# Kernel optimization log

Hardware: AMD Instinct MI355X
Metric: run time of the kernel (lower is better)

The kernel has to match this reference:

```python
import jax, jax.numpy as jnp
import numpy as np

V, E, H, T = 50000, 300, 512, 16   # vocab, embed_dim, hidden_dim, tagset
Hh = H // 2                         # per-direction LSTM hidden
B, S = 128, 128                     # batch (hardcoded in module), seq_len
START, STOP = 14, 15
NEG = -10000.0


def setup_inputs() -> dict:
    key = jax.random.key(0)
    ks = jax.random.split(key, 16)
    n = lambda k, sh: (jax.random.normal(k, sh, dtype=jnp.float32) * 0.1)
    trans = jax.random.normal(ks[12], (T, T), dtype=jnp.float32)
    trans = trans.at[START, :].set(NEG).at[:, STOP].set(NEG)
    return {
        "sentence": jax.random.randint(ks[0], (B, S), 0, V, dtype=jnp.int32),
        "emb": jax.random.normal(ks[1], (V, E), dtype=jnp.float32),
        "Wih_f": n(ks[2], (4 * Hh, E)), "Whh_f": n(ks[3], (4 * Hh, Hh)),
        "bih_f": n(ks[4], (4 * Hh,)),   "bhh_f": n(ks[5], (4 * Hh,)),
        "Wih_b": n(ks[6], (4 * Hh, E)), "Whh_b": n(ks[7], (4 * Hh, Hh)),
        "bih_b": n(ks[8], (4 * Hh,)),   "bhh_b": n(ks[9], (4 * Hh,)),
        "W_out": n(ks[10], (T, H)),     "b_out": n(ks[11], (T,)),
        "trans": trans,
        "h0": jax.random.normal(ks[13], (2, B, Hh), dtype=jnp.float32),
        "c0": jax.random.normal(ks[14], (2, B, Hh), dtype=jnp.float32),
    }


def _lstm_dir(x_sbE, h0, c0, Wih, Whh, bih, bhh):
    """x_sbE: [S,B,E] -> [S,B,Hh]. PyTorch gate order: i,f,g,o."""
    def cell(carry, xt):
        h, c = carry
        g = xt @ Wih.T + bih + h @ Whh.T + bhh
        i, f, gg, o = jnp.split(g, 4, axis=-1)
        c = jax.nn.sigmoid(f) * c + jax.nn.sigmoid(i) * jnp.tanh(gg)
        h = jax.nn.sigmoid(o) * jnp.tanh(c)
        return (h, c), h
    _, hs = jax.lax.scan(cell, (h0, c0), x_sbE)
    return hs


def _viterbi(feats, trans):
    """Batched Viterbi. feats: [B,S,T]. Returns (scores [B], paths [B,S])."""
    init = jnp.full((B, T), NEG, dtype=feats.dtype).at[:, START].set(0.0)

    def step(fv, feat_t):
        # next_tag_var[b, next, prev] = fv[b, prev] + trans[next, prev]
        nxt = fv[:, None, :] + trans[None, :, :]
        bp = jnp.argmax(nxt, axis=-1)              # [B,T]
        fv = jnp.max(nxt, axis=-1) + feat_t        # [B,T]
        return fv, bp

    fv, bps = jax.lax.scan(step, init, jnp.swapaxes(feats, 0, 1))  # bps: [S,B,T]
    term = fv + trans[STOP][None, :]
    best = jnp.argmax(term, axis=-1)               # [B]
    score = jnp.max(term, axis=-1)                 # [B]

    def back(tag, bp_t):
        prev = jnp.take_along_axis(bp_t, tag[:, None], axis=1)[:, 0]
        return prev, tag

    _, path = jax.lax.scan(back, best, bps, reverse=True)  # [S,B]
    return score, jnp.swapaxes(path, 0, 1)


def reference(sentence, emb, Wih_f, Whh_f, bih_f, bhh_f,
              Wih_b, Whh_b, bih_b, bhh_b, W_out, b_out, trans, h0, c0):
    x = emb[sentence]                               # [B,S,E] (frozen embedding)
    x_sbE = jnp.swapaxes(x, 0, 1)                   # [S,B,E]
    h_f = _lstm_dir(x_sbE, h0[0], c0[0], Wih_f, Whh_f, bih_f, bhh_f)
    h_b = _lstm_dir(x_sbE[::-1], h0[1], c0[1], Wih_b, Whh_b, bih_b, bhh_b)[::-1]
    lstm_out = jnp.concatenate([h_f, h_b], axis=-1)  # [S,B,H]
    feats = jnp.swapaxes(lstm_out @ W_out.T + b_out, 0, 1)  # [B,S,T]
    scores, tag_seqs = _viterbi(feats, trans)
    return scores, tag_seqs
```

## Files before the change

### kernel.cpp

```cpp
#include <hip/hip_runtime.h>
#include <math.h>
#include <stdint.h>

#define BB 128
#define SS 128
#define EE 300
#define HH 256
#define G4 1024
#define TT 16
#define NEGV -10000.0f
#define START_TAG 14
#define STOP_TAG 15

typedef float f32x4 __attribute__((ext_vector_type(4)));

__device__ __forceinline__ float sigm(float x) { return 1.0f / (1.0f + expf(-x)); }

__device__ __forceinline__ float4 shfl_xor4(float4 v, int m) {
  float4 r;
  r.x = __shfl_xor(v.x, m); r.y = __shfl_xor(v.y, m);
  r.z = __shfl_xor(v.z, m); r.w = __shfl_xor(v.w, m);
  return r;
}
__device__ __forceinline__ void add4(float4& a, const float4& b) {
  a.x += b.x; a.y += b.y; a.z += b.z; a.w += b.w;
}

__device__ __forceinline__ void load_pairs8(const float* p, f32x4& a, f32x4& b) {
  asm volatile("global_load_dwordx4 %0, %2, off sc0 sc1\n\t"
               "global_load_dwordx4 %1, %2, off offset:16 sc0 sc1\n\t"
               "s_waitcnt vmcnt(0)"
               : "=&v"(a), "=&v"(b) : "v"(p) : "memory");
}

__device__ __forceinline__ void store_pair_llc(float2* p, float h, int stamp) {
  uint64_t bits = ((uint64_t)(uint32_t)stamp << 32) | (uint64_t)__float_as_uint(h);
  __hip_atomic_store((uint64_t*)p, bits, __ATOMIC_RELAXED, __HIP_MEMORY_SCOPE_AGENT);
}

__global__ void k_prep(const float* __restrict__ Wih_f, const float* __restrict__ Whh_f,
                       const float* __restrict__ bih_f, const float* __restrict__ bhh_f,
                       const float* __restrict__ Wih_b, const float* __restrict__ Whh_b,
                       const float* __restrict__ bih_b, const float* __restrict__ bhh_b,
                       float* __restrict__ WihT, float* __restrict__ Whh4,
                       float* __restrict__ bsum, float* __restrict__ hpairz) {
  int id = blockIdx.x * blockDim.x + threadIdx.x;
  const int N1 = 2 * EE * G4;
  const int N2 = 2 * HH * G4;
  const int N3 = 2 * G4;
  const int N4 = 3 * 2 * BB * HH * 2;
  if (id < N1) {
    int d = id / (EE * G4); int r = id % (EE * G4);
    int e = r / G4; int j = r % G4;
    const float* W = d ? Wih_b : Wih_f;
    WihT[id] = W[j * EE + e];
  } else if (id < N1 + N2) {
    int t = id - N1;
    int d = t / (HH * G4); int r = t % (HH * G4);
    int k = r / G4; int q = r % G4; int u = q >> 2; int g = q & 3;
    const float* W = d ? Whh_b : Whh_f;
    Whh4[t] = W[(g * HH + u) * HH + k];
  } else if (id < N1 + N2 + N3) {
    int t = id - N1 - N2;
    int d = t / G4; int j = t % G4;
    bsum[t] = d ? (bih_b[j] + bhh_b[j]) : (bih_f[j] + bhh_f[j]);
  } else if (id < N1 + N2 + N3 + N4) {
    hpairz[id - N1 - N2 - N3] = 0.0f;
  }
}

__global__ void k_xproj(const int* __restrict__ sent, const float* __restrict__ emb,
                        const float* __restrict__ WihT, const float* __restrict__ bsum,
                        float4* __restrict__ xp4) {
  __shared__ __align__(16) float xs[16][EE];
  __shared__ int idxs[16];
  int blk = blockIdx.x;
  int d = blk >> 10;
  int tile = blk & 1023;
  int tid = threadIdx.x;
  if (tid < 16) {
    int sb = tile * 16 + tid;
    int s = sb >> 7, b = sb & 127;
    idxs[tid] = sent[b * SS + s];
  }
  __syncthreads();
  for (int t = tid; t < 16 * 75; t += 256) {
    int i = t / 75, e4 = t % 75;
    ((f32x4*)&xs[i][0])[e4] = ((const f32x4*)(emb + (size_t)idxs[i] * EE))[e4];
  }
  __syncthreads();

  const float* WT = WihT + (size_t)d * EE * G4;
  float acc0[16], acc1[16], acc2[16], acc3[16];
#pragma unroll
  for (int i = 0; i < 16; ++i) { acc0[i] = 0.f; acc1[i] = 0.f; acc2[i] = 0.f; acc3[i] = 0.f; }

  for (int e4 = 0; e4 < 75; ++e4) {
    f32x4 xv[16];
#pragma unroll
    for (int i = 0; i < 16; ++i)
      xv[i] = *(const f32x4*)&xs[i][e4 * 4];
    const float* rowb = WT + (size_t)e4 * 4 * G4;
#pragma unroll
    for (int j = 0; j < 4; ++j) {
      const float* row = rowb + (size_t)j * G4;
      float w0 = row[tid];
      float w1 = row[tid + 256];
      float w2 = row[tid + 512];
      float w3 = row[tid + 768];
#pragma unroll
      for (int i = 0; i < 16; ++i) {
        float x = xv[i][j];
        acc0[i] += w0 * x; acc1[i] += w1 * x; acc2[i] += w2 * x; acc3[i] += w3 * x;
      }
    }
  }
  float b0 = bsum[d * G4 + tid];
  float b1 = bsum[d * G4 + tid + 256];
  float b2 = bsum[d * G4 + tid + 512];
  float b3 = bsum[d * G4 + tid + 768];
#pragma unroll
  for (int i = 0; i < 16; ++i) {
    int sb = tile * 16 + i;
    int s = sb >> 7, b = sb & 127;
    xp4[(((size_t)d * SS + s) * BB + b) * HH + tid] =
        make_float4(acc0[i] + b0, acc1[i] + b1, acc2[i] + b2, acc3[i] + b3);
  }
}

__global__ __launch_bounds__(256, 2) void k_recur(
    const float4* __restrict__ xp4, const float4* __restrict__ Wg,
    const float* __restrict__ h0, const float* __restrict__ c0,
    float2* __restrict__ hpair, float* __restrict__ hall) {
  __shared__ __align__(16) float hsh[2][4 * 288];

  int blk = blockIdx.x;
  int d = blk >> 8;
  int bg = (blk >> 3) & 31;
  int sl = blk & 7;
  int bbase = bg * 4;
  int tid = threadIdx.x;
  int u = tid >> 3, kc = tid & 7;
  int uglob = sl * 32 + u;

  float4 wreg[32];
  {
    const float4* Wd = Wg + (size_t)d * (HH * HH) + (size_t)(kc * 32) * HH + uglob;
#pragma unroll
    for (int kk = 0; kk < 32; ++kk) wreg[kk] = Wd[(size_t)kk * HH];
  }
  int b_own = ((kc & 1) << 1) | ((kc >> 1) & 1);
  float c_reg = c0[((size_t)d * BB + bbase + b_own) * HH + uglob];
  bool up0 = (kc & 1), up1 = (kc & 2);

  int sb = tid >> 6;
  int k4 = (tid & 63) * 4;
  int ldoff = sb * 288 + (k4 >> 5) * 36 + (k4 & 31);

  for (int step = 0; step < SS; ++step) {
    int s = d ? (SS - 1 - step) : step;
    int pb = step & 1;
    float4 xg = xp4[(((size_t)d * SS + s) * BB + bbase + b_own) * HH + uglob];

    float* ldst = &hsh[pb][ldoff];
    if (step == 0) {
      const float* ps = h0 + ((size_t)d * BB + bbase + sb) * HH + k4;
      *(f32x4*)ldst = *(const f32x4*)ps;
    } else {
      int slot_r = (step + 2) % 3;
      const float* ps = (const float*)(hpair +
          ((size_t)(slot_r * 2 + d) * BB + bbase + sb) * HH + k4);
      f32x4 v0, v1;
      load_pairs8(ps, v0, v1);
      while (__float_as_int(v0[1]) != step || __float_as_int(v0[3]) != step ||
             __float_as_int(v1[1]) != step || __float_as_int(v1[3]) != step) {
        __builtin_amdgcn_s_sleep(1);
        load_pairs8(ps, v0, v1);
      }
      f32x4 q = {v0[0], v0[2], v1[0], v1[2]};
      *(f32x4*)ldst = q;
    }
    __syncthreads();

    const float* hb = &hsh[pb][0];
    float4 a[4];
#pragma unroll
    for (int b = 0; b < 4; ++b) a[b] = make_float4(0.f, 0.f, 0.f, 0.f);
#pragma unroll
    for (int kk4 = 0; kk4 < 8; ++kk4) {
      float hvv[4][4];
#pragma unroll
      for (int b = 0; b < 4; ++b)
        *(f32x4*)&hvv[b][0] = *(const f32x4*)&hb[b * 288 + kc * 36 + kk4 * 4];
#pragma unroll
      for (int j = 0; j < 4; ++j) {
        float4 w = wreg[kk4 * 4 + j];
#pragma unroll
        for (int b = 0; b < 4; ++b) {
          float hj = hvv[b][j];
          a[b].x += w.x * hj; a[b].y += w.y * hj;
          a[b].z += w.z * hj; a[b].w += w.w * hj;
        }
      }
    }

#pragma unroll
    for (int j = 0; j < 2; ++j) {
      float4 snd = up0 ? a[j] : a[j + 2];
      float4 rcv = shfl_xor4(snd, 1);
      if (!up0) add4(a[j], rcv); else add4(a[j + 2], rcv);
    }
    float4 v0 = up0 ? a[2] : a[0];
    float4 v1 = up0 ? a[3] : a[1];
    {
      float4 snd = up1 ? v0 : v1;
      float4 rcv = shfl_xor4(snd, 2);
      if (!up1) add4(v0, rcv); else add4(v1, rcv);
    }
    float4 keep = up1 ? v1 : v0;
    {
      float4 rcv = shfl_xor4(keep, 4);
      add4(keep, rcv);
    }

    float ii = keep.x + xg.x, ff = keep.y + xg.y;
    float gg = keep.z + xg.z, oo = keep.w + xg.w;
    c_reg = sigm(ff) * c_reg + sigm(ii) * tanhf(gg);
    float hn = sigm(oo) * tanhf(c_reg);

    if (kc < 4) {
      store_pair_llc(&hpair[((size_t)((step % 3) * 2 + d) * BB + bbase + b_own) * HH + uglob],
                     hn, step + 1);
      hall[(((size_t)d * SS + step) * BB + bbase + b_own) * HH + uglob] = hn;
    }
  }
}

__global__ void k_feats(const float* __restrict__ hall, const float* __restrict__ Wout,
                        float* __restrict__ featsF) {
  __shared__ __align__(16) float h2[16][516];
  int b = blockIdx.x >> 3;
  int sg = blockIdx.x & 7;
  int tid = threadIdx.x;

  for (int i = tid; i < 16 * 128; i += 256) {
    int r = i >> 7, seg = i & 127;
    int s = sg * 16 + r;
    f32x4 v;
    if (seg < 64)
      v = *(const f32x4*)&hall[(((size_t)0 * SS + s) * BB + b) * HH + seg * 4];
    else
      v = *(const f32x4*)&hall[(((size_t)1 * SS + (SS - 1 - s)) * BB + b) * HH + (seg - 64) * 4];
    *(f32x4*)&h2[r][seg * 4] = v;
  }
  __syncthreads();

  int sloc = tid >> 4, t = tid & 15;
  const float* wrow = Wout + t * 512;
  float p = 0.f;
  for (int j = 0; j < 128; ++j) {
    f32x4 hv = *(const f32x4*)&h2[sloc][j * 4];
    f32x4 wv = *(const f32x4*)&wrow[j * 4];
    p += hv[0] * wv[0] + hv[1] * wv[1] + hv[2] * wv[2] + hv[3] * wv[3];
  }
  featsF[((size_t)b * SS + sg * 16 + sloc) * TT + t] = p;
}

__global__ void k_viterbi(const float* __restrict__ featsF, const float* __restrict__ b_out,
                          const float* __restrict__ trans, float* __restrict__ out) {
  __shared__ float tr[TT * TT];
  __shared__ unsigned char bpl[16][SS][TT];
  int tid = threadIdx.x;
  if (tid < TT * TT) tr[tid] = trans[tid];
  __syncthreads();

  int bg = tid >> 4;
  int next = tid & 15;
  int b = blockIdx.x * 16 + bg;
  float fv = (next == START_TAG) ? 0.0f : NEGV;
  float bo = b_out[next];
  const float* fF = featsF + (size_t)b * SS * TT;

  for (int s = 0; s < SS; ++s) {
    float best = -INFINITY; int arg = 0;
#pragma unroll
    for (int prev = 0; prev < TT; ++prev) {
      float fvp = __shfl(fv, prev, 16);
      float cand = fvp + tr[next * TT + prev];
      if (cand > best) { best = cand; arg = prev; }
    }
    float feat = fF[s * TT + next] + bo;
    fv = best + feat;
    bpl[bg][s][next] = (unsigned char)arg;
  }

  float bv = fv + tr[STOP_TAG * TT + next];
  int bi = next;
#pragma unroll
  for (int off = 8; off; off >>= 1) {
    float ov = __shfl_down(bv, off, 16);
    int oi = __shfl_down(bi, off, 16);
    if (ov > bv || (ov == bv && oi < bi)) { bv = ov; bi = oi; }
  }
  if (next == 0) {
    out[b] = bv;
    int tag = bi;
    float* po = out + BB + (size_t)b * SS;
    for (int s = SS - 1; s >= 0; --s) {
      po[s] = (float)tag;
      tag = bpl[bg][s][tag];
    }
  }
}

extern "C" void kernel_launch(void* const* d_in, const int* in_sizes, int n_in,
                              void* d_out, int out_size, void* d_ws, size_t ws_size,
                              hipStream_t stream) {
  const int*   sent  = (const int*)d_in[0];
  const float* emb   = (const float*)d_in[1];
  const float* Wih_f = (const float*)d_in[2];
  const float* Whh_f = (const float*)d_in[3];
  const float* bih_f = (const float*)d_in[4];
  const float* bhh_f = (const float*)d_in[5];
  const float* Wih_b = (const float*)d_in[6];
  const float* Whh_b = (const float*)d_in[7];
  const float* bih_b = (const float*)d_in[8];
  const float* bhh_b = (const float*)d_in[9];
  const float* Wout  = (const float*)d_in[10];
  const float* b_out = (const float*)d_in[11];
  const float* trans = (const float*)d_in[12];
  const float* h0    = (const float*)d_in[13];
  const float* c0    = (const float*)d_in[14];

  float* ws = (float*)d_ws;
  size_t off = 0;
  float* xproj  = ws + off; off += (size_t)2 * SS * BB * G4;
  float* WihT   = ws + off; off += (size_t)2 * EE * G4;
  float* Whh4   = ws + off; off += (size_t)2 * HH * G4;
  float* bsum   = ws + off; off += (size_t)2 * G4;
  float* featsF = ws + off; off += (size_t)BB * SS * TT;
  float* hall   = ws + off; off += (size_t)2 * SS * BB * HH;
  float* hpairf = ws + off; off += (size_t)3 * 2 * BB * HH * 2;

  const int NPREP = 2 * EE * G4 + 2 * HH * G4 + 2 * G4 + 3 * 2 * BB * HH * 2;
  k_prep<<<(NPREP + 255) / 256, 256, 0, stream>>>(Wih_f, Whh_f, bih_f, bhh_f,
                                                  Wih_b, Whh_b, bih_b, bhh_b,
                                                  WihT, Whh4, bsum, hpairf);
  k_xproj<<<2048, 256, 0, stream>>>(sent, emb, WihT, bsum, (float4*)xproj);

  {
    const float4* xp4c = (const float4*)xproj;
    const float4* Wgc  = (const float4*)Whh4;
    float2* hpair = (float2*)hpairf;
    void* kargs[] = {(void*)&xp4c, (void*)&Wgc, (void*)&h0, (void*)&c0,
                     (void*)&hpair, (void*)&hall};
    hipError_t e = hipLaunchCooperativeKernel(k_recur, dim3(512), dim3(256),
                                              kargs, 0, stream);
    if (e != hipSuccess) {
      k_recur<<<512, 256, 0, stream>>>(xp4c, Wgc, h0, c0, hpair, hall);
    }
  }

  k_feats<<<1024, 256, 0, stream>>>(hall, Wout, featsF);
  k_viterbi<<<8, 256, 0, stream>>>(featsF, b_out, trans, (float*)d_out);
}
```

Before: 909.0 us.

## Fuse input projection into recurrence kernel with per-row stamp flags for overlap

Merges the embedding/input-projection kernel into the persistent recurrence kernel as extra worker blocks, so projection of later timesteps overlaps the sequential LSTM recurrence. The recurrence blocks spin on per-(step,batch,slice) ready flags written by the projection blocks and read the projected gates with cache-bypassing loads. Projection tiles shrink to 8 rows and are ordered by time per direction. The aim is to hide the projection GEMM's latency behind the recurrence. The cost is extra flag polling, the loss of the cooperative launch guarantee of co-residency, and a risk of deadlock if recurrence blocks occupy the GPU before the projection blocks are scheduled.

Result: slower. 3.416 ms (+275.7%).

```diff
diff --git a/kernel.cpp b/kernel.cpp
--- a/kernel.cpp
+++ b/kernel.cpp
@@ -11,6 +11,8 @@
 #define NEGV -10000.0f
 #define START_TAG 14
 #define STOP_TAG 15
+#define NRB 512
+#define NXB 4096
 
 typedef float f32x4 __attribute__((ext_vector_type(4)));
 
@@ -32,9 +34,26 @@
                "s_waitcnt vmcnt(0)"
                : "=&v"(a), "=&v"(b) : "v"(p) : "memory");
 }
-
+__device__ __forceinline__ f32x4 load_f4_llc(const float* p) {
+  f32x4 v;
+  asm volatile("global_load_dwordx4 %0, %1, off sc0 sc1\n\t"
+               "s_waitcnt vmcnt(0)"
+               : "=v"(v) : "v"(p) : "memory");
+  return v;
+}
+__device__ __forceinline__ int load_int_llc(const int* p) {
+  int v;
+  asm volatile("global_load_dword %0, %1, off sc0 sc1\n\t"
+               "s_waitcnt vmcnt(0)"
+               : "=v"(v) : "v"(p) : "memory");
+  return v;
+}
 __device__ __forceinline__ void store_pair_llc(float2* p, float h, int stamp) {
   uint64_t bits = ((uint64_t)(uint32_t)stamp << 32) | (uint64_t)__float_as_uint(h);
+  __hip_atomic_store((uint64_t*)p, bits, __ATOMIC_RELAXED, __HIP_MEMORY_SCOPE_AGENT);
+}
+__device__ __forceinline__ void store_f2_llc(float* p, float a, float b) {
+  uint64_t bits = ((uint64_t)__float_as_uint(b) << 32) | (uint64_t)__float_as_uint(a);
   __hip_atomic_store((uint64_t*)p, bits, __ATOMIC_RELAXED, __HIP_MEMORY_SCOPE_AGENT);
 }
 
@@ -43,12 +62,14 @@
                        const float* __restrict__ Wih_b, const float* __restrict__ Whh_b,
                        const float* __restrict__ bih_b, const float* __restrict__ bhh_b,
                        float* __restrict__ WihT, float* __restrict__ Whh4,
-                       float* __restrict__ bsum, float* __restrict__ hpairz) {
+                       float* __restrict__ bsum, float* __restrict__ hpairz,
+                       int* __restrict__ xstamp) {
   int id = blockIdx.x * blockDim.x + threadIdx.x;
   const int N1 = 2 * EE * G4;
   const int N2 = 2 * HH * G4;
   const int N3 = 2 * G4;
   const int N4 = 3 * 2 * BB * HH * 2;
+  const int N5 = 2 * SS * BB * 8;
   if (id < N1) {
     int d = id / (EE * G4); int r = id % (EE * G4);
     int e = r / G4; int j = r % G4;
@@ -66,172 +87,186 @@
     bsum[t] = d ? (bih_b[j] + bhh_b[j]) : (bih_f[j] + bhh_f[j]);
   } else if (id < N1 + N2 + N3 + N4) {
     hpairz[id - N1 - N2 - N3] = 0.0f;
-  }
-}
-
-__global__ void k_xproj(const int* __restrict__ sent, const float* __restrict__ emb,
-                        const float* __restrict__ WihT, const float* __restrict__ bsum,
-                        float4* __restrict__ xp4) {
-  __shared__ __align__(16) float xs[16][EE];
-  __shared__ int idxs[16];
-  int blk = blockIdx.x;
-  int d = blk >> 10;
-  int tile = blk & 1023;
-  int tid = threadIdx.x;
-  if (tid < 16) {
-    int sb = tile * 16 + tid;
-    int s = sb >> 7, b = sb & 127;
-    idxs[tid] = sent[b * SS + s];
-  }
-  __syncthreads();
-  for (int t = tid; t < 16 * 75; t += 256) {
-    int i = t / 75, e4 = t % 75;
-    ((f32x4*)&xs[i][0])[e4] = ((const f32x4*)(emb + (size_t)idxs[i] * EE))[e4];
-  }
-  __syncthreads();
-
-  const float* WT = WihT + (size_t)d * EE * G4;
-  float acc0[16], acc1[16], acc2[16], acc3[16];
-#pragma unroll
-  for (int i = 0; i < 16; ++i) { acc0[i] = 0.f; acc1[i] = 0.f; acc2[i] = 0.f; acc3[i] = 0.f; }
-
-  for (int e4 = 0; e4 < 75; ++e4) {
-    f32x4 xv[16];
-#pragma unroll
-    for (int i = 0; i < 16; ++i)
-      xv[i] = *(const f32x4*)&xs[i][e4 * 4];
-    const float* rowb = WT + (size_t)e4 * 4 * G4;
-#pragma unroll
-    for (int j = 0; j < 4; ++j) {
-      const float* row = rowb + (size_t)j * G4;
-      float w0 = row[tid];
-      float w1 = row[tid + 256];
-      float w2 = row[tid + 512];
-      float w3 = row[tid + 768];
-#pragma unroll
-      for (int i = 0; i < 16; ++i) {
-        float x = xv[i][j];
-        acc0[i] += w0 * x; acc1[i] += w1 * x; acc2[i] += w2 * x; acc3[i] += w3 * x;
-      }
-    }
-  }
-  float b0 = bsum[d * G4 + tid];
-  float b1 = bsum[d * G4 + tid + 256];
-  float b2 = bsum[d * G4 + tid + 512];
-  float b3 = bsum[d * G4 + tid + 768];
-#pragma unroll
-  for (int i = 0; i < 16; ++i) {
-    int sb = tile * 16 + i;
-    int s = sb >> 7, b = sb & 127;
-    xp4[(((size_t)d * SS + s) * BB + b) * HH + tid] =
-        make_float4(acc0[i] + b0, acc1[i] + b1, acc2[i] + b2, acc3[i] + b3);
-  }
-}
-
-__global__ __launch_bounds__(256, 2) void k_recur(
-    const float4* __restrict__ xp4, const float4* __restrict__ Wg,
-    const float* __restrict__ h0, const float* __restrict__ c0,
-    float2* __restrict__ hpair, float* __restrict__ hall) {
-  __shared__ __align__(16) float hsh[2][4 * 288];
-
-  int blk = blockIdx.x;
-  int d = blk >> 8;
-  int bg = (blk >> 3) & 31;
-  int sl = blk & 7;
-  int bbase = bg * 4;
-  int tid = threadIdx.x;
-  int u = tid >> 3, kc = tid & 7;
-  int uglob = sl * 32 + u;
-
-  float4 wreg[32];
-  {
-    const float4* Wd = Wg + (size_t)d * (HH * HH) + (size_t)(kc * 32) * HH + uglob;
-#pragma unroll
-    for (int kk = 0; kk < 32; ++kk) wreg[kk] = Wd[(size_t)kk * HH];
-  }
-  int b_own = ((kc & 1) << 1) | ((kc >> 1) & 1);
-  float c_reg = c0[((size_t)d * BB + bbase + b_own) * HH + uglob];
-  bool up0 = (kc & 1), up1 = (kc & 2);
-
-  int sb = tid >> 6;
-  int k4 = (tid & 63) * 4;
-  int ldoff = sb * 288 + (k4 >> 5) * 36 + (k4 & 31);
-
-  for (int step = 0; step < SS; ++step) {
-    int s = d ? (SS - 1 - step) : step;
-    int pb = step & 1;
-    float4 xg = xp4[(((size_t)d * SS + s) * BB + bbase + b_own) * HH + uglob];
-
-    float* ldst = &hsh[pb][ldoff];
-    if (step == 0) {
-      const float* ps = h0 + ((size_t)d * BB + bbase + sb) * HH + k4;
-      *(f32x4*)ldst = *(const f32x4*)ps;
-    } else {
-      int slot_r = (step + 2) % 3;
-      const float* ps = (const float*)(hpair +
-          ((size_t)(slot_r * 2 + d) * BB + bbase + sb) * HH + k4);
-      f32x4 v0, v1;
-      load_pairs8(ps, v0, v1);
-      while (__float_as_int(v0[1]) != step || __float_as_int(v0[3]) != step ||
-             __float_as_int(v1[1]) != step || __float_as_int(v1[3]) != step) {
-        __builtin_amdgcn_s_sleep(1);
+  } else if (id < N1 + N2 + N3 + N4 + N5) {
+    xstamp[id - N1 - N2 - N3 - N4] = 0;
+  }
+}
+
+__global__ __launch_bounds__(256, 4) void k_main(
+    const float4* __restrict__ Wg, const float* __restrict__ h0,
+    const float* __restrict__ c0, float2* __restrict__ hpair,
+    float* __restrict__ hall, float* __restrict__ xp4, int* __restrict__ xstamp,
+    const int* __restrict__ sent, const float* __restrict__ emb,
+    const float* __restrict__ WihT, const float* __restrict__ bsum) {
+  __shared__ __align__(16) float smem[2432];
+  __shared__ int idxs[8];
+  int blk = blockIdx.x, tid = threadIdx.x;
+
+  if (blk < NRB) {
+    int d = blk >> 8, bg = (blk >> 3) & 31, sl = blk & 7;
+    int bbase = bg * 4;
+    int u = tid >> 3, kc = tid & 7;
+    int uglob = sl * 32 + u;
+
+    float4 wreg[32];
+    {
+      const float4* Wd = Wg + (size_t)d * (HH * HH) + (size_t)(kc * 32) * HH + uglob;
+#pragma unroll
+      for (int kk = 0; kk < 32; ++kk) wreg[kk] = Wd[(size_t)kk * HH];
+    }
+    int b_own = ((kc & 1) << 1) | ((kc >> 1) & 1);
+    float c_reg = c0[((size_t)d * BB + bbase + b_own) * HH + uglob];
+    bool up0 = (kc & 1), up1 = (kc & 2);
+
+    int sb = tid >> 6;
+    int k4 = (tid & 63) * 4;
+    int ldoff = sb * 288 + (k4 >> 5) * 36 + (k4 & 31);
+
+    for (int step = 0; step < SS; ++step) {
+      int s = d ? (SS - 1 - step) : step;
+      int pb = step & 1;
+
+      float4 xg;
+      {
+        const int* sp = xstamp + ((size_t)(d * SS + s) * BB + bbase + b_own) * 8 + sl;
+        while (load_int_llc(sp) != 1) __builtin_amdgcn_s_sleep(8);
+        f32x4 xv = load_f4_llc(xp4 + ((size_t)(d * SS + s) * BB + bbase + b_own) * G4 +
+                               uglob * 4);
+        xg = make_float4(xv[0], xv[1], xv[2], xv[3]);
+      }
+
+      float* ldst = &smem[pb * 1152 + ldoff];
+      if (step == 0) {
+        const float* ps = h0 + ((size_t)d * BB + bbase + sb) * HH + k4;
+        *(f32x4*)ldst = *(const f32x4*)ps;
+      } else {
+        int slot_r = (step + 2) % 3;
+        const float* ps = (const float*)(hpair +
+            ((size_t)(slot_r * 2 + d) * BB + bbase + sb) * HH + k4);
+        f32x4 v0, v1;
         load_pairs8(ps, v0, v1);
-      }
-      f32x4 q = {v0[0], v0[2], v1[0], v1[2]};
-      *(f32x4*)ldst = q;
+        while (__float_as_int(v0[1]) != step || __float_as_int(v0[3]) != step ||
+               __float_as_int(v1[1]) != step || __float_as_int(v1[3]) != step) {
+          __builtin_amdgcn_s_sleep(1);
+          load_pairs8(ps, v0, v1);
+        }
+        f32x4 q = {v0[0], v0[2], v1[0], v1[2]};
+        *(f32x4*)ldst = q;
+      }
+      __syncthreads();
+
+      const float* hb = &smem[pb * 1152];
+      float4 a[4];
+#pragma unroll
+      for (int b = 0; b < 4; ++b) a[b] = make_float4(0.f, 0.f, 0.f, 0.f);
+#pragma unroll
+      for (int kk4 = 0; kk4 < 8; ++kk4) {
+        float hvv[4][4];
+#pragma unroll
+        for (int b = 0; b < 4; ++b)
+          *(f32x4*)&hvv[b][0] = *(const f32x4*)&hb[b * 288 + kc * 36 + kk4 * 4];
+#pragma unroll
+        for (int j = 0; j < 4; ++j) {
+          float4 w = wreg[kk4 * 4 + j];
+#pragma unroll
+          for (int b = 0; b < 4; ++b) {
+            float hj = hvv[b][j];
+            a[b].x += w.x * hj; a[b].y += w.y * hj;
+            a[b].z += w.z * hj; a[b].w += w.w * hj;
+          }
+        }
+      }
+
+#pragma unroll
+      for (int j = 0; j < 2; ++j) {
+        float4 snd = up0 ? a[j] : a[j + 2];
+        float4 rcv = shfl_xor4(snd, 1);
+        if (!up0) add4(a[j], rcv); else add4(a[j + 2], rcv);
+      }
+      float4 v0 = up0 ? a[2] : a[0];
+      float4 v1 = up0 ? a[3] : a[1];
+      {
+        float4 snd = up1 ? v0 : v1;
+        float4 rcv = shfl_xor4(snd, 2);
+        if (!up1) add4(v0, rcv); else add4(v1, rcv);
+      }
+      float4 keep = up1 ? v1 : v0;
+      {
+        float4 rcv = shfl_xor4(keep, 4);
+        add4(keep, rcv);
+      }
+
+      float ii = keep.x + xg.x, ff = keep.y + xg.y;
+      float gg = keep.z + xg.z, oo = keep.w + xg.w;
+      c_reg = sigm(ff) * c_reg + sigm(ii) * tanhf(gg);
+      float hn = sigm(oo) * tanhf(c_reg);
+
+      if (kc < 4) {
+        store_pair_llc(&hpair[((size_t)((step % 3) * 2 + d) * BB + bbase + b_own) * HH + uglob],
+                       hn, step + 1);
+        hall[(((size_t)d * SS + step) * BB + bbase + b_own) * HH + uglob] = hn;
+      }
+    }
+  } else {
+    int xb = blk - NRB;
+    int d = xb & 1;
+    int t = d ? (2047 - (xb >> 1)) : (xb >> 1);
+
+    if (tid < 8) {
+      int sb = t * 8 + tid;
+      int s = sb >> 7, b = sb & 127;
+      idxs[tid] = sent[b * SS + s];
     }
     __syncthreads();
-
-    const float* hb = &hsh[pb][0];
-    float4 a[4];
-#pragma unroll
-    for (int b = 0; b < 4; ++b) a[b] = make_float4(0.f, 0.f, 0.f, 0.f);
-#pragma unroll
-    for (int kk4 = 0; kk4 < 8; ++kk4) {
-      float hvv[4][4];
-#pragma unroll
-      for (int b = 0; b < 4; ++b)
-        *(f32x4*)&hvv[b][0] = *(const f32x4*)&hb[b * 288 + kc * 36 + kk4 * 4];
+    for (int i = tid; i < 8 * 75; i += 256) {
+      int r = i / 75, e4 = i % 75;
+      *(f32x4*)&smem[r * 300 + e4 * 4] = ((const f32x4*)(emb + (size_t)idxs[r] * EE))[e4];
+    }
+    __syncthreads();
+
+    const float* WT = WihT + (size_t)d * EE * G4;
+    float acc0[8], acc1[8], acc2[8], acc3[8];
+#pragma unroll
+    for (int i = 0; i < 8; ++i) { acc0[i] = 0.f; acc1[i] = 0.f; acc2[i] = 0.f; acc3[i] = 0.f; }
+
+    for (int e4 = 0; e4 < 75; ++e4) {
+      f32x4 xv[8];
+#pragma unroll
+      for (int i = 0; i < 8; ++i) xv[i] = *(const f32x4*)&smem[i * 300 + e4 * 4];
+      const float* rowb = WT + (size_t)e4 * 4 * G4;
 #pragma unroll
       for (int j = 0; j < 4; ++j) {
-        float4 w = wreg[kk4 * 4 + j];
-#pragma unroll
-        for (int b = 0; b < 4; ++b) {
-          float hj = hvv[b][j];
-          a[b].x += w.x * hj; a[b].y += w.y * hj;
-          a[b].z += w.z * hj; a[b].w += w.w * hj;
+        const float* row = rowb + (size_t)j * G4;
+        float w0 = row[tid];
+        float w1 = row[tid + 256];
+        float w2 = row[tid + 512];
+        float w3 = row[tid + 768];
+#pragma unroll
+        for (int i = 0; i < 8; ++i) {
+          float x = xv[i][j];
+          acc0[i] += w0 * x; acc1[i] += w1 * x; acc2[i] += w2 * x; acc3[i] += w3 * x;
         }
       }
     }
-
-#pragma unroll
-    for (int j = 0; j < 2; ++j) {
-      float4 snd = up0 ? a[j] : a[j + 2];
-      float4 rcv = shfl_xor4(snd, 1);
-      if (!up0) add4(a[j], rcv); else add4(a[j + 2], rcv);
-    }
-    float4 v0 = up0 ? a[2] : a[0];
-    float4 v1 = up0 ? a[3] : a[1];
-    {
-      float4 snd = up1 ? v0 : v1;
-      float4 rcv = shfl_xor4(snd, 2);
-      if (!up1) add4(v0, rcv); else add4(v1, rcv);
-    }
-    float4 keep = up1 ? v1 : v0;
-    {
-      float4 rcv = shfl_xor4(keep, 4);
-      add4(keep, rcv);
-    }
-
-    float ii = keep.x + xg.x, ff = keep.y + xg.y;
-    float gg = keep.z + xg.z, oo = keep.w + xg.w;
-    c_reg = sigm(ff) * c_reg + sigm(ii) * tanhf(gg);
-    float hn = sigm(oo) * tanhf(c_reg);
-
-    if (kc < 4) {
-      store_pair_llc(&hpair[((size_t)((step % 3) * 2 + d) * BB + bbase + b_own) * HH + uglob],
-                     hn, step + 1);
-      hall[(((size_t)d * SS + step) * BB + bbase + b_own) * HH + uglob] = hn;
+    float b0 = bsum[d * G4 + tid];
+    float b1 = bsum[d * G4 + tid + 256];
+    float b2 = bsum[d * G4 + tid + 512];
+    float b3 = bsum[d * G4 + tid + 768];
+#pragma unroll
+    for (int i = 0; i < 8; ++i) {
+      int sb = t * 8 + i;
+      int s = sb >> 7, b = sb & 127;
+      float* base = xp4 + ((size_t)(d * SS + s) * BB + b) * G4 + tid * 4;
+      store_f2_llc(base, acc0[i] + b0, acc1[i] + b1);
+      store_f2_llc(base + 2, acc2[i] + b2, acc3[i] + b3);
+    }
+    __syncthreads();
+    if (tid < 64) {
+      int r = tid >> 3, sl = tid & 7;
+      int sb = t * 8 + r;
+      int s = sb >> 7, b = sb & 127;
+      __hip_atomic_store(xstamp + ((size_t)(d * SS + s) * BB + b) * 8 + sl, 1,
+                         __ATOMIC_RELAXED, __HIP_MEMORY_SCOPE_AGENT);
     }
   }
 }
@@ -334,7 +369,8 @@
 
   float* ws = (float*)d_ws;
   size_t off = 0;
-  float* xproj  = ws + off; off += (size_t)2 * SS * BB * G4;
+  float* xp4    = ws + off; off += (size_t)2 * SS * BB * G4;
+  int*   xstamp = (int*)(ws + off); off += (size_t)2 * SS * BB * 8;
   float* WihT   = ws + off; off += (size_t)2 * EE * G4;
   float* Whh4   = ws + off; off += (size_t)2 * HH * G4;
   float* bsum   = ws + off; off += (size_t)2 * G4;
@@ -342,24 +378,15 @@
   float* hall   = ws + off; off += (size_t)2 * SS * BB * HH;
   float* hpairf = ws + off; off += (size_t)3 * 2 * BB * HH * 2;
 
-  const int NPREP = 2 * EE * G4 + 2 * HH * G4 + 2 * G4 + 3 * 2 * BB * HH * 2;
+  const int NPREP = 2 * EE * G4 + 2 * HH * G4 + 2 * G4 +
+                    3 * 2 * BB * HH * 2 + 2 * SS * BB * 8;
   k_prep<<<(NPREP + 255) / 256, 256, 0, stream>>>(Wih_f, Whh_f, bih_f, bhh_f,
                                                   Wih_b, Whh_b, bih_b, bhh_b,
-                                                  WihT, Whh4, bsum, hpairf);
-  k_xproj<<<2048, 256, 0, stream>>>(sent, emb, WihT, bsum, (float4*)xproj);
-
-  {
-    const float4* xp4c = (const float4*)xproj;
-    const float4* Wgc  = (const float4*)Whh4;
-    float2* hpair = (float2*)hpairf;
-    void* kargs[] = {(void*)&xp4c, (void*)&Wgc, (void*)&h0, (void*)&c0,
-                     (void*)&hpair, (void*)&hall};
-    hipError_t e = hipLaunchCooperativeKernel(k_recur, dim3(512), dim3(256),
-                                              kargs, 0, stream);
-    if (e != hipSuccess) {
-      k_recur<<<512, 256, 0, stream>>>(xp4c, Wgc, h0, c0, hpair, hall);
-    }
-  }
+                                                  WihT, Whh4, bsum, hpairf, xstamp);
+
+  k_main<<<NRB + NXB, 256, 0, stream>>>((const float4*)Whh4, h0, c0,
+                                        (float2*)hpairf, hall, xp4, xstamp,
+                                        sent, emb, WihT, bsum);
 
   k_feats<<<1024, 256, 0, stream>>>(hall, Wout, featsF);
   k_viterbi<<<8, 256, 0, stream>>>(featsF, b_out, trans, (float*)d_out);
```
